# Kernel tuning notes

Measured on AMD Instinct MI355X. Metric: run time of the kernel, lower is better.

Reference implementation:

```python
import jax, jax.numpy as jnp
import numpy as np

KH, KW = 2, 2  # kernel_size; stride == kernel_size (default), pad == 0 for this config

def setup_inputs() -> dict:
    key = jax.random.key(0)
    k1, k2 = jax.random.split(key)
    B, C, H, W = 32, 64, 64, 64
    nH, nW = H // KH, W // KW
    L = nH * nW                     # 1024
    n = KH * KW * C                 # 256 (grouping = in_feature)
    x = jax.random.normal(k1, (B, C, H, W), dtype=jnp.float32)
    stdv = 6.0 / np.sqrt(n * n / 1.0) ** 0.5  # placeholder, recomputed below
    stdv = 6.0 / np.sqrt(float(n * n) / 1.0) if False else 6.0 / np.sqrt(float(n) * float(n) / float(n)) / 1.0
    stdv = 6.0 / np.sqrt(float(n * n))  # numel // L == n*n -> stdv = 6/sqrt(n*n) = 6/n
    weight = jax.random.uniform(k2, (L, n, n), dtype=jnp.float32, minval=-stdv, maxval=stdv)
    bias = jnp.zeros((1, 1, n, L), dtype=jnp.float32)
    return {"x": x, "weight": weight, "bias": bias}

def reference(x, weight, bias):
    # PointConv with kernel=(2,2), stride=(2,2), pad=0, grouping=C.
    B, C, H, W = x.shape
    nH, nW = H // KH, W // KW
    L = nH * nW
    n = C * KH * KW
    # F.unfold (non-overlapping, stride==kernel): channel order (c, kh, kw), L order (ph, pw)
    patches = x.reshape(B, C, nH, KH, nW, KW).transpose(0, 1, 3, 5, 2, 4).reshape(B, n, L)
    p = patches.reshape(B, 1, n, L)  # (B, C//grouping=1, n, L)
    # per-location matmul: distinct [n,n] weight per spatial patch l
    m = jnp.einsum('bcnl,lnp->bcpl', p, weight) + bias  # (B,1,n,L)
    m = m.reshape(B, C, KH, KW, nH, nW)
    # F.fold inverse of the unfold above
    out = m.transpose(0, 1, 4, 2, 5, 3).reshape(B, C, H, W)
    return out
```

## Files before the change

kernel.cpp:

```cpp
#include <hip/hip_runtime.h>


#define B_  32
#define C_  64
#define H_  64
#define W_  64
#define L_  1024
#define N_  256
#define SA  264
#define PW  268

typedef __bf16 bf16x8 __attribute__((ext_vector_type(8)));
typedef float  f32x4  __attribute__((ext_vector_type(4)));

__device__ __forceinline__ unsigned short f2bf(float f) {
  unsigned int u = __builtin_bit_cast(unsigned int, f);
  u += 0x7FFFu + ((u >> 16) & 1u);
  return (unsigned short)(u >> 16);
}

__global__ __launch_bounds__(256, 3) void pointconv_kernel(
    const float* __restrict__ x, const float* __restrict__ wgt,
    const float* __restrict__ bias, float* __restrict__ out) {
  __shared__ unsigned short A[B_ * SA];
  __shared__ unsigned short WS[32 * PW];

  const int bid = blockIdx.x;
  const int l  = ((bid & 7) << 7) | (bid >> 3);
  const int ph = l >> 5, pw = l & 31;
  const int h0 = ph * 2, w0 = pw * 2;
  const int tid = threadIdx.x;

  const float* __restrict__ wl = wgt + (size_t)l * (N_ * N_);

  const int kb = (tid >> 6) * 8;
  const int pq = (tid & 63) * 4;
  const float* wbase = wl + kb * N_ + pq;

  f32x4 wreg[8];
#pragma unroll
  for (int i = 0; i < 8; ++i)
    wreg[i] = *(const f32x4*)(wbase + i * N_);

  {
    const int b  = tid & 31;
    const int c0 = tid >> 5;
#pragma unroll
    for (int i = 0; i < 8; ++i) {
      const int c = c0 + i * 8;
      const float* px = x + (((b * C_ + c) * H_ + h0) * W_ + w0);
      float2 v0 = *(const float2*)px;
      float2 v1 = *(const float2*)(px + W_);
      ushort4 q;
      q.x = f2bf(v0.x); q.y = f2bf(v0.y);
      q.z = f2bf(v1.x); q.w = f2bf(v1.y);
      *(ushort4*)&A[b * SA + c * 4] = q;
    }
  }

  const int lane = tid & 63;
  const int wv   = tid >> 6;
  const int col  = lane & 15;
  const int quad = lane >> 4;

  f32x4 acc[2][4];
#pragma unroll
  for (int nt = 0; nt < 4; ++nt) {
    const int p = wv * 64 + nt * 16 + col;
    const float bv = bias[p * L_ + l];
#pragma unroll
    for (int mt = 0; mt < 2; ++mt) {
      acc[mt][nt][0] = bv; acc[mt][nt][1] = bv;
      acc[mt][nt][2] = bv; acc[mt][nt][3] = bv;
    }
  }

#pragma unroll 1
  for (int k0 = 0; k0 < N_; k0 += 32) {
#pragma unroll
    for (int i = 0; i < 8; ++i) {
      ushort4 q;
      q.x = f2bf(wreg[i][0]); q.y = f2bf(wreg[i][1]);
      q.z = f2bf(wreg[i][2]); q.w = f2bf(wreg[i][3]);
      *(ushort4*)&WS[(kb + i) * PW + pq] = q;
    }
    __syncthreads();

    if (k0 + 32 < N_) {
      const float* nb = wbase + (k0 + 32) * N_;
#pragma unroll
      for (int i = 0; i < 8; ++i)
        wreg[i] = *(const f32x4*)(nb + i * N_);
    }

    bf16x8 af[2];
#pragma unroll
    for (int mt = 0; mt < 2; ++mt)
      af[mt] = *(const bf16x8*)&A[(mt * 16 + col) * SA + k0 + quad * 8];

#pragma unroll
    for (int nt = 0; nt < 4; ++nt) {
      const int p = wv * 64 + nt * 16 + col;
      union { unsigned short s[8]; bf16x8 v; } bu;
#pragma unroll
      for (int j = 0; j < 8; ++j)
        bu.s[j] = WS[(quad * 8 + j) * PW + p];
#pragma unroll
      for (int mt = 0; mt < 2; ++mt)
        acc[mt][nt] = __builtin_amdgcn_mfma_f32_16x16x32_bf16(
            af[mt], bu.v, acc[mt][nt], 0, 0, 0);
    }
    __syncthreads();
  }

#pragma unroll
  for (int mt = 0; mt < 2; ++mt) {
#pragma unroll
    for (int nt = 0; nt < 4; ++nt) {
      const int p  = wv * 64 + nt * 16 + col;
      const int c  = p >> 2;
      const int kh = (p >> 1) & 1;
      const int kw = p & 1;
      float* po = out + (((c * H_) + h0 + kh) * W_ + w0 + kw);
#pragma unroll
      for (int r = 0; r < 4; ++r) {
        const int b = mt * 16 + quad * 4 + r;
        po[b * (C_ * H_ * W_)] = acc[mt][nt][r];
      }
    }
  }
}

extern "C" void kernel_launch(void* const* d_in, const int* in_sizes, int n_in,
                              void* d_out, int out_size, void* d_ws, size_t ws_size,
                              hipStream_t stream) {
  const float* x    = (const float*)d_in[0];
  const float* wgt  = (const float*)d_in[1];
  const float* bias = (const float*)d_in[2];
  float* out = (float*)d_out;
  pointconv_kernel<<<dim3(L_), dim3(256), 0, stream>>>(x, wgt, bias, out);
}
```

Before: 417.7 us.

## Double-buffer weight tiles in registers and LDS with prefetch distance two

```diff
diff --git a/kernel.cpp b/kernel.cpp
--- a/kernel.cpp
+++ b/kernel.cpp
@@ -23,7 +23,7 @@
     const float* __restrict__ x, const float* __restrict__ wgt,
     const float* __restrict__ bias, float* __restrict__ out) {
   __shared__ unsigned short A[B_ * SA];
-  __shared__ unsigned short WS[32 * PW];
+  __shared__ unsigned short WS[2][32 * PW];
 
   const int bid = blockIdx.x;
   const int l  = ((bid & 7) << 7) | (bid >> 3);
@@ -37,10 +37,11 @@
   const int pq = (tid & 63) * 4;
   const float* wbase = wl + kb * N_ + pq;
 
-  f32x4 wreg[8];
+  f32x4 wreg[2][8];
 #pragma unroll
-  for (int i = 0; i < 8; ++i)
-    wreg[i] = *(const f32x4*)(wbase + i * N_);
+  for (int i = 0; i < 8; ++i) wreg[0][i] = *(const f32x4*)(wbase + i * N_);
+#pragma unroll
+  for (int i = 0; i < 8; ++i) wreg[1][i] = *(const f32x4*)(wbase + (32 + i) * N_);
 
   {
     const int b  = tid & 31;
@@ -75,22 +76,24 @@
     }
   }
 
+#pragma unroll
+  for (int i = 0; i < 8; ++i) {
+    ushort4 q;
+    q.x = f2bf(wreg[0][i][0]); q.y = f2bf(wreg[0][i][1]);
+    q.z = f2bf(wreg[0][i][2]); q.w = f2bf(wreg[0][i][3]);
+    *(ushort4*)&WS[0][(kb + i) * PW + pq] = q;
+  }
+  __syncthreads();
+
 #pragma unroll 1
-  for (int k0 = 0; k0 < N_; k0 += 32) {
+  for (int it = 0; it < 8; ++it) {
+    const int buf = it & 1;
+    const int k0  = it * 32;
+
+    if (it + 2 < 8) {
+      const float* nb = wbase + (it + 2) * 32 * N_;
 #pragma unroll
-    for (int i = 0; i < 8; ++i) {
-      ushort4 q;
-      q.x = f2bf(wreg[i][0]); q.y = f2bf(wreg[i][1]);
-      q.z = f2bf(wreg[i][2]); q.w = f2bf(wreg[i][3]);
-      *(ushort4*)&WS[(kb + i) * PW + pq] = q;
-    }
-    __syncthreads();
-
-    if (k0 + 32 < N_) {
-      const float* nb = wbase + (k0 + 32) * N_;
-#pragma unroll
-      for (int i = 0; i < 8; ++i)
-        wreg[i] = *(const f32x4*)(nb + i * N_);
+      for (int i = 0; i < 8; ++i) wreg[buf][i] = *(const f32x4*)(nb + i * N_);
     }
 
     bf16x8 af[2];
@@ -98,17 +101,28 @@
     for (int mt = 0; mt < 2; ++mt)
       af[mt] = *(const bf16x8*)&A[(mt * 16 + col) * SA + k0 + quad * 8];
 
+    const unsigned short* ws = WS[buf];
 #pragma unroll
     for (int nt = 0; nt < 4; ++nt) {
       const int p = wv * 64 + nt * 16 + col;
       union { unsigned short s[8]; bf16x8 v; } bu;
 #pragma unroll
       for (int j = 0; j < 8; ++j)
-        bu.s[j] = WS[(quad * 8 + j) * PW + p];
+        bu.s[j] = ws[(quad * 8 + j) * PW + p];
 #pragma unroll
       for (int mt = 0; mt < 2; ++mt)
         acc[mt][nt] = __builtin_amdgcn_mfma_f32_16x16x32_bf16(
             af[mt], bu.v, acc[mt][nt], 0, 0, 0);
+    }
+
+    if (it + 1 < 8) {
+#pragma unroll
+      for (int i = 0; i < 8; ++i) {
+        ushort4 q;
+        q.x = f2bf(wreg[buf ^ 1][i][0]); q.y = f2bf(wreg[buf ^ 1][i][1]);
+        q.z = f2bf(wreg[buf ^ 1][i][2]); q.w = f2bf(wreg[buf ^ 1][i][3]);
+        *(ushort4*)&WS[buf ^ 1][(kb + i) * PW + pq] = q;
+      }
     }
     __syncthreads();
   }
```

Result: slower. 480.7 us (+15.1%).
